# Kernel tuning notes

Hardware: AMD Instinct MI355X
Metric: run time of the kernel (lower is better)

Reference implementation:

```python
import jax, jax.numpy as jnp
import numpy as np

N_HEADS = 16
ROPE_BASE = 10000.0

def apply_rope(x):
    # x: [B, H, S, D] with D even; interleaved-pair RoPE (torchtune style)
    B, H, S, D = x.shape
    half = D // 2
    inv_freq = 1.0 / (ROPE_BASE ** (jnp.arange(0, half, dtype=jnp.float32) / half))
    angles = jnp.arange(S, dtype=jnp.float32)[:, None] * inv_freq[None, :]  # [S, D/2]
    cos = jnp.cos(angles)[None, None]  # [1,1,S,D/2]
    sin = jnp.sin(angles)[None, None]
    x1 = x[..., 0::2]
    x2 = x[..., 1::2]
    r1 = x1 * cos - x2 * sin
    r2 = x1 * sin + x2 * cos
    return jnp.stack([r1, r2], axis=-1).reshape(B, H, S, D)

def setup_inputs() -> dict:
    key = jax.random.key(0)
    ks = jax.random.split(key, 5)
    B, S, E = 2, 2048, 1024
    d_attn = 1024
    scale = 1.0 / np.sqrt(E)
    x = jax.random.normal(ks[0], (B, S, E), dtype=jnp.float32)
    Wq = jax.random.normal(ks[1], (d_attn, E), dtype=jnp.float32) * scale
    Wk = jax.random.normal(ks[2], (d_attn, E), dtype=jnp.float32) * scale
    Wv = jax.random.normal(ks[3], (d_attn, E), dtype=jnp.float32) * scale
    Wo = jax.random.normal(ks[4], (E, d_attn), dtype=jnp.float32) * scale
    return {"x": x, "Wq": Wq, "Wk": Wk, "Wv": Wv, "Wo": Wo}

def reference(x, Wq, Wk, Wv, Wo):
    B, S, E = x.shape
    d_attn = Wq.shape[0]
    hd = d_attn // N_HEADS
    attn_scale = 1.0 / np.sqrt(d_attn)
    # projections (nn.Linear: x @ W.T), split heads -> [B, H, S, hd]
    q = (x @ Wq.T).reshape(B, S, N_HEADS, hd).transpose(0, 2, 1, 3)
    k = (x @ Wk.T).reshape(B, S, N_HEADS, hd).transpose(0, 2, 1, 3)
    v = (x @ Wv.T).reshape(B, S, N_HEADS, hd).transpose(0, 2, 1, 3)
    q = apply_rope(q)
    k = apply_rope(k)
    scores = jnp.einsum('bhqd,bhkd->bhqk', q, k) * attn_scale  # [B,H,S,S]
    causal = jnp.tril(jnp.ones((S, S), dtype=bool))
    scores = jnp.where(causal[None, None], scores, -jnp.inf)
    probs = jax.nn.softmax(scores, axis=-1)  # dropout is identity in eval
    out = jnp.einsum('bhqk,bhkd->bhqd', probs, v)
    out = out.transpose(0, 2, 1, 3).reshape(B, S, d_attn)
    return out @ Wo.T
```

## Files before the change

### kernel.cpp

```cpp
#include <hip/hip_runtime.h>


typedef float  f32x4  __attribute__((ext_vector_type(4)));
typedef short  short8 __attribute__((ext_vector_type(8)));

#define MFMA16(a,b,c) __builtin_amdgcn_mfma_f32_16x16x32_bf16((a),(b),(c),0,0,0)
#define GLD_LDS16(g, l)                                                        \
  __builtin_amdgcn_global_load_lds(                                            \
      (const __attribute__((address_space(1))) unsigned int*)(g),              \
      (__attribute__((address_space(3))) unsigned int*)(l), 16, 0, 0)

__device__ __forceinline__ unsigned short f2bf(float f) {
  unsigned int x = __float_as_uint(f);
  x += 0x7fffu + ((x >> 16) & 1u);
  return (unsigned short)(x >> 16);
}
__device__ __forceinline__ float bf2f(unsigned short u) {
  return __uint_as_float(((unsigned int)u) << 16);
}

__global__ __launch_bounds__(256) void cvt_all(const float* __restrict__ x,
                                               const float* __restrict__ wq,
                                               const float* __restrict__ wk,
                                               const float* __restrict__ wv,
                                               const float* __restrict__ wo,
                                               ushort* __restrict__ dst) {
  const int i = blockIdx.x * 256 + threadIdx.x;
  const float* src;
  int off;
  if (i < 1048576) { src = x; off = i; }
  else {
    const int j = i - 1048576;
    const int wsel = j >> 18;
    off = j & 262143;
    src = (wsel == 0) ? wq : (wsel == 1) ? wk : (wsel == 2) ? wv : wo;
  }
  const float4 v = ((const float4*)src)[off];
  ushort4 o = make_ushort4(f2bf(v.x), f2bf(v.y), f2bf(v.z), f2bf(v.w));
  ((ushort4*)dst)[i] = o;
}

template<int MODE, int BN, int BM>
__global__ __launch_bounds__(256) void gemm_bt(const ushort* __restrict__ A,
                                               const ushort* __restrict__ B,
                                               void* __restrict__ Cv,
                                               int K) {
  constexpr int NI = BN / 32;
  constexpr int MI = BM / 32;
  constexpr int AI = BM / 64;
  constexpr int BI = BN / 64;
  __shared__ __align__(16) short As0[BM * 32];
  __shared__ __align__(16) short As1[BM * 32];
  __shared__ __align__(16) short Bs0[BN * 32];
  __shared__ __align__(16) short Bs1[BN * 32];
  const int tid  = threadIdx.x;
  const int lane = tid & 63, w = tid >> 6;
  const int ln   = lane & 15, quad = lane >> 4;
  const int wm   = w >> 1, wn = w & 1;
  const int m0 = blockIdx.y * BM, n0 = blockIdx.x * BN;

  const int srow = lane >> 2;
  const int schk = (lane & 3) * 8;
  const int arow = w * (16 * AI);
  const int brow = w * (16 * BI);
  const ushort* Ag0 = A + (size_t)(m0 + arow + srow) * K + schk;
  const ushort* Ag1 = A + (size_t)(m0 + arow + 16 + srow) * K + schk;
  const ushort* Bg0 = B + (size_t)(n0 + brow + srow) * K + schk;
  const ushort* Bg1 = B + (size_t)(n0 + brow + 16 + srow) * K + schk;
  const int lA0 = arow * 32, lA1 = (arow + 16) * 32;
  const int lB0 = brow * 32, lB1 = (brow + 16) * 32;

  int aoff[MI], boff[NI];
#pragma unroll
  for (int i = 0; i < MI; i++)
    aoff[i] = (wm * (BM / 2) + i * 16 + ln) * 32 + quad * 8;
#pragma unroll
  for (int i = 0; i < NI; i++)
    boff[i] = (wn * (BN / 2) + i * 16 + ln) * 32 + quad * 8;
  f32x4 acc[MI][NI] = {};

  for (int kt = 0; kt < K; kt += 64) {
    __syncthreads();
    GLD_LDS16(Ag0 + kt, As0 + lA0);
    if (AI == 2) GLD_LDS16(Ag1 + kt, As0 + lA1);
    GLD_LDS16(Ag0 + kt + 32, As1 + lA0);
    if (AI == 2) GLD_LDS16(Ag1 + kt + 32, As1 + lA1);
    GLD_LDS16(Bg0 + kt, Bs0 + lB0);
    if (BI == 2) GLD_LDS16(Bg1 + kt, Bs0 + lB1);
    GLD_LDS16(Bg0 + kt + 32, Bs1 + lB0);
    if (BI == 2) GLD_LDS16(Bg1 + kt + 32, Bs1 + lB1);
    __syncthreads();
#pragma unroll
    for (int h = 0; h < 2; ++h) {
      const short* Ap = h ? As1 : As0;
      const short* Bp = h ? Bs1 : Bs0;
      short8 av[MI], bv[NI];
#pragma unroll
      for (int i = 0; i < MI; i++) av[i] = *(const short8*)&Ap[aoff[i]];
#pragma unroll
      for (int i = 0; i < NI; i++) bv[i] = *(const short8*)&Bp[boff[i]];
#pragma unroll
      for (int mi = 0; mi < MI; mi++)
#pragma unroll
        for (int ni = 0; ni < NI; ni++)
          acc[mi][ni] = MFMA16(av[mi], bv[ni], acc[mi][ni]);
    }
  }

  if (MODE == 0) {
    ushort* Cq = (ushort*)Cv;
    if (n0 < 2048) {
      ushort* dst = Cq + (n0 < 1024 ? 0 : 4194304);
      const int nbase = (n0 < 1024) ? n0 : n0 - 1024;
      const float qsc = (n0 < 1024) ? 0.04508422002778011f : 1.0f;
      const float sgn = (ln & 1) ? 1.0f : -1.0f;
      float invc[NI];
#pragma unroll
      for (int ni = 0; ni < NI; ni++) {
        const int ii = ((wn * (BN / 2) + ni * 16 + ln) & 63) >> 1;
        invc[ni] = __builtin_amdgcn_exp2f(-(float)ii * 0.4152410118579865f) *
                   0.15915494309189535f;
      }
#pragma unroll
      for (int mi = 0; mi < MI; mi++) {
        const int row = m0 + wm * (BM / 2) + mi * 16 + quad * 4;
#pragma unroll
        for (int ni = 0; ni < NI; ni++) {
          const int col = nbase + wn * (BN / 2) + ni * 16 + ln;
#pragma unroll
          for (int r = 0; r < 4; r++) {
            const float mine  = acc[mi][ni][r];
            const float other = __shfl_xor(mine, 1, 64);
            const int   s     = (row + r) & 2047;
            const float rev   = (float)s * invc[ni];
            const float rr    = rev - floorf(rev);
            const float sn = __builtin_amdgcn_sinf(rr);
            const float cs = __builtin_amdgcn_cosf(rr);
            const float rot = (mine * cs + sgn * other * sn) * qsc;
            dst[(size_t)(row + r) * 1024 + col] = f2bf(rot);
          }
        }
      }
    } else {
      ushort* vt = Cq + 8388608;
#pragma unroll
      for (int mi = 0; mi < MI; mi++) {
        const int sm = m0 + wm * (BM / 2) + mi * 16 + quad * 4;
        const int b = sm >> 11, s = sm & 2047;
#pragma unroll
        for (int ni = 0; ni < NI; ni++) {
          const int nv = (n0 - 2048) + wn * (BN / 2) + ni * 16 + ln;
          const int bh = b * 16 + (nv >> 6), d = nv & 63;
          ushort4 u = make_ushort4(f2bf(acc[mi][ni][0]), f2bf(acc[mi][ni][1]),
                                   f2bf(acc[mi][ni][2]), f2bf(acc[mi][ni][3]));
          *(ushort4*)&vt[((size_t)bh * 64 + d) * 2048 + s] = u;
        }
      }
    }
  } else {
    float* C = (float*)Cv;
#pragma unroll
    for (int mi = 0; mi < MI; mi++) {
      const int row = m0 + wm * (BM / 2) + mi * 16 + quad * 4;
#pragma unroll
      for (int ni = 0; ni < NI; ni++) {
        const int col = n0 + wn * (BN / 2) + ni * 16 + ln;
#pragma unroll
        for (int r = 0; r < 4; r++)
          C[(size_t)(row + r) * 1024 + col] = acc[mi][ni][r];
      }
    }
  }
}

__global__ __launch_bounds__(256) void attnk(const ushort* __restrict__ q,
                                             const ushort* __restrict__ k,
                                             const ushort* __restrict__ vt,
                                             ushort* __restrict__ ctx) {
  __shared__ __align__(16) short Ks[64 * 72];
  __shared__ __align__(16) short Vs[64 * 72];
  __shared__ __align__(16) short Ps[4 * 16 * 72];
  const int tid  = threadIdx.x;
  const int lane = tid & 63, w = tid >> 6;
  const int ln   = lane & 15, quad = lane >> 4;
  const int x = blockIdx.x, bh = blockIdx.y;
  const int b = bh >> 4, h = bh & 15;
  const int jA = x, jB = 31 - x;
  short* Pw = Ps + w * 1152;

  const size_t qbA = ((size_t)(b * 2048 + jA * 64 + w * 16 + ln)) * 1024 + h * 64;
  const size_t qbB = ((size_t)(b * 2048 + jB * 64 + w * 16 + ln)) * 1024 + h * 64;
  const short8 aqA0 = *(const short8*)&q[qbA + quad * 8];
  const short8 aqA1 = *(const short8*)&q[qbA + 32 + quad * 8];
  const short8 aqB0 = *(const short8*)&q[qbB + quad * 8];
  const short8 aqB1 = *(const short8*)&q[qbB + 32 + quad * 8];

  f32x4 oA[4] = {}, oB[4] = {};
  float lsA[4] = {0.f, 0.f, 0.f, 0.f}, lsB[4] = {0.f, 0.f, 0.f, 0.f};

  const int s0 = tid, s1 = tid + 256;
  const int r0 = s0 >> 3, c0 = (s0 & 7) * 8;
  const int r1 = s1 >> 3, c1 = (s1 & 7) * 8;
  const ushort* kg0 = k  + ((size_t)(b * 2048 + r0)) * 1024 + h * 64 + c0;
  const ushort* kg1 = k  + ((size_t)(b * 2048 + r1)) * 1024 + h * 64 + c1;
  const ushort* vg0 = vt + ((size_t)(bh * 64 + r0)) * 2048 + c0;
  const ushort* vg1 = vt + ((size_t)(bh * 64 + r1)) * 2048 + c1;
  const int wK0 = r0 * 72 + c0, wK1 = r1 * 72 + c1;

  for (int t = 0; t <= jB; t++) {
    __syncthreads();
    *(short8*)&Ks[wK0] = *(const short8*)(kg0 + (size_t)t * 65536);
    *(short8*)&Ks[wK1] = *(const short8*)(kg1 + (size_t)t * 65536);
    *(short8*)&Vs[wK0] = *(const short8*)(vg0 + t * 64);
    *(short8*)&Vs[wK1] = *(const short8*)(vg1 + t * 64);
    __syncthreads();

    const bool actA = (t <= jA);
    f32x4 scA[4], scB[4];
#pragma unroll
    for (int ct = 0; ct < 4; ct++) {
      const short8 bk0 = *(const short8*)&Ks[(ct * 16 + ln) * 72 + quad * 8];
      const short8 bk1 = *(const short8*)&Ks[(ct * 16 + ln) * 72 + 32 + quad * 8];
      f32x4 z = {0.f, 0.f, 0.f, 0.f};
      z = MFMA16(aqB0, bk0, z);
      z = MFMA16(aqB1, bk1, z);
      scB[ct] = z;
      if (actA) {
        f32x4 y = {0.f, 0.f, 0.f, 0.f};
        y = MFMA16(aqA0, bk0, y);
        y = MFMA16(aqA1, bk1, y);
        scA[ct] = y;
      }
    }
    if (t == jB) {
#pragma unroll
      for (int ct = 0; ct < 4; ct++) {
        const int kv = (t << 6) + ct * 16 + ln;
#pragma unroll
        for (int r = 0; r < 4; r++)
          if (kv > jB * 64 + w * 16 + quad * 4 + r) scB[ct][r] = -100000.0f;
      }
    }
    if (actA && t == jA) {
#pragma unroll
      for (int ct = 0; ct < 4; ct++) {
        const int kv = (t << 6) + ct * 16 + ln;
#pragma unroll
        for (int r = 0; r < 4; r++)
          if (kv > jA * 64 + w * 16 + quad * 4 + r) scA[ct][r] = -100000.0f;
      }
    }

    short8 bv0[4], bv1[4];
#pragma unroll
    for (int dt = 0; dt < 4; dt++) {
      bv0[dt] = *(const short8*)&Vs[(dt * 16 + ln) * 72 + quad * 8];
      bv1[dt] = *(const short8*)&Vs[(dt * 16 + ln) * 72 + 32 + quad * 8];
    }

#pragma unroll
    for (int ct = 0; ct < 4; ct++)
#pragma unroll
      for (int r = 0; r < 4; r++) {
        const float p = __builtin_amdgcn_exp2f(scB[ct][r]);
        lsB[r] += p;
        Pw[(quad * 4 + r) * 72 + ct * 16 + ln] = (short)f2bf(p);
      }
    {
      const short8 ap0 = *(const short8*)&Pw[ln * 72 + quad * 8];
      const short8 ap1 = *(const short8*)&Pw[ln * 72 + 32 + quad * 8];
#pragma unroll
      for (int dt = 0; dt < 4; dt++) {
        oB[dt] = MFMA16(ap0, bv0[dt], oB[dt]);
        oB[dt] = MFMA16(ap1, bv1[dt], oB[dt]);
      }
    }
    if (actA) {
#pragma unroll
      for (int ct = 0; ct < 4; ct++)
#pragma unroll
        for (int r = 0; r < 4; r++) {
          const float p = __builtin_amdgcn_exp2f(scA[ct][r]);
          lsA[r] += p;
          Pw[(quad * 4 + r) * 72 + ct * 16 + ln] = (short)f2bf(p);
        }
      const short8 ap0 = *(const short8*)&Pw[ln * 72 + quad * 8];
      const short8 ap1 = *(const short8*)&Pw[ln * 72 + 32 + quad * 8];
#pragma unroll
      for (int dt = 0; dt < 4; dt++) {
        oA[dt] = MFMA16(ap0, bv0[dt], oA[dt]);
        oA[dt] = MFMA16(ap1, bv1[dt], oA[dt]);
      }
    }
  }

#pragma unroll
  for (int off = 1; off < 16; off <<= 1)
#pragma unroll
    for (int r = 0; r < 4; r++) {
      lsA[r] += __shfl_xor(lsA[r], off, 64);
      lsB[r] += __shfl_xor(lsB[r], off, 64);
    }

#pragma unroll
  for (int r = 0; r < 4; r++) {
    const float invA = 1.0f / lsA[r];
    const float invB = 1.0f / lsB[r];
    const int rowA = jA * 64 + w * 16 + quad * 4 + r;
    const int rowB = jB * 64 + w * 16 + quad * 4 + r;
#pragma unroll
    for (int dt = 0; dt < 4; dt++) {
      ctx[((size_t)(b * 2048 + rowA)) * 1024 + h * 64 + dt * 16 + ln] =
          f2bf(oA[dt][r] * invA);
      ctx[((size_t)(b * 2048 + rowB)) * 1024 + h * 64 + dt * 16 + ln] =
          f2bf(oB[dt][r] * invB);
    }
  }
}

extern "C" void kernel_launch(void* const* d_in, const int* in_sizes, int n_in,
                              void* d_out, int out_size, void* d_ws, size_t ws_size,
                              hipStream_t stream) {
  const float* x  = (const float*)d_in[0];
  const float* Wq = (const float*)d_in[1];
  const float* Wk = (const float*)d_in[2];
  const float* Wv = (const float*)d_in[3];
  const float* Wo = (const float*)d_in[4];
  float* out = (float*)d_out;
  char* ws = (char*)d_ws;

  ushort* xb  = (ushort*)(ws);
  ushort* wqb = (ushort*)(ws + (size_t)(8  << 20));
  ushort* qb  = (ushort*)(ws + (size_t)(16 << 20));
  ushort* kb  = (ushort*)(ws + (size_t)(24 << 20));
  ushort* vtb = (ushort*)(ws + (size_t)(32 << 20));
  ushort* ctx = (ushort*)(ws + (size_t)(40 << 20));

  cvt_all<<<8192, 256, 0, stream>>>(x, Wq, Wk, Wv, Wo, xb);
  gemm_bt<0, 64, 128><<<dim3(48, 32), 256, 0, stream>>>(xb, wqb, (void*)qb, 1024);
  attnk<<<dim3(16, 32), 256, 0, stream>>>(qb, kb, vtb, ctx);
  gemm_bt<2, 64, 64><<<dim3(16, 64), 256, 0, stream>>>(ctx, wqb + 3145728 , (void*)out, 1024);
}
```

Baseline: 190.8 us.

## Split attention query tiles across 8 waves with double-buffered K/V staging

The attention kernel now launches 512 threads per block, and each group of 4 waves owns one of the two paired query tiles, where before every wave processed both tiles in turn. K/V tiles are double-buffered in LDS and prefetched two steps ahead through registers, which removes one barrier per iteration. QK^T is computed transposed so probabilities pack into bf16 pairs with v_cvt_pk_bf16 and vector LDS stores, and the row-sum reduction needs fewer shuffles. The cost is more LDS per block and idle waves in the short tile during later iterations.

```diff
diff --git a/kernel.cpp b/kernel.cpp
--- a/kernel.cpp
+++ b/kernel.cpp
@@ -17,6 +17,11 @@
 }
 __device__ __forceinline__ float bf2f(unsigned short u) {
   return __uint_as_float(((unsigned int)u) << 16);
+}
+__device__ __forceinline__ unsigned int cvtpk_bf16(float lo, float hi) {
+  unsigned int r;
+  asm("v_cvt_pk_bf16_f32 %0, %1, %2" : "=v"(r) : "v"(lo), "v"(hi));
+  return r;
 }
 
 __global__ __launch_bounds__(256) void cvt_all(const float* __restrict__ x,
@@ -173,147 +178,120 @@
   }
 }
 
-__global__ __launch_bounds__(256) void attnk(const ushort* __restrict__ q,
+__global__ __launch_bounds__(512) void attnk(const ushort* __restrict__ q,
                                              const ushort* __restrict__ k,
                                              const ushort* __restrict__ vt,
                                              ushort* __restrict__ ctx) {
-  __shared__ __align__(16) short Ks[64 * 72];
-  __shared__ __align__(16) short Vs[64 * 72];
-  __shared__ __align__(16) short Ps[4 * 16 * 72];
+  __shared__ __align__(16) short Ks[2][64 * 72];
+  __shared__ __align__(16) short Vs[2][64 * 72];
+  __shared__ __align__(16) short Ps[8 * 16 * 72];
   const int tid  = threadIdx.x;
   const int lane = tid & 63, w = tid >> 6;
   const int ln   = lane & 15, quad = lane >> 4;
   const int x = blockIdx.x, bh = blockIdx.y;
   const int b = bh >> 4, h = bh & 15;
   const int jA = x, jB = 31 - x;
+  const int tile = w >> 2;
+  const int wq   = w & 3;
+  const int j    = tile ? jA : jB;
   short* Pw = Ps + w * 1152;
 
-  const size_t qbA = ((size_t)(b * 2048 + jA * 64 + w * 16 + ln)) * 1024 + h * 64;
-  const size_t qbB = ((size_t)(b * 2048 + jB * 64 + w * 16 + ln)) * 1024 + h * 64;
-  const short8 aqA0 = *(const short8*)&q[qbA + quad * 8];
-  const short8 aqA1 = *(const short8*)&q[qbA + 32 + quad * 8];
-  const short8 aqB0 = *(const short8*)&q[qbB + quad * 8];
-  const short8 aqB1 = *(const short8*)&q[qbB + 32 + quad * 8];
-
-  f32x4 oA[4] = {}, oB[4] = {};
-  float lsA[4] = {0.f, 0.f, 0.f, 0.f}, lsB[4] = {0.f, 0.f, 0.f, 0.f};
-
-  const int s0 = tid, s1 = tid + 256;
-  const int r0 = s0 >> 3, c0 = (s0 & 7) * 8;
-  const int r1 = s1 >> 3, c1 = (s1 & 7) * 8;
-  const ushort* kg0 = k  + ((size_t)(b * 2048 + r0)) * 1024 + h * 64 + c0;
-  const ushort* kg1 = k  + ((size_t)(b * 2048 + r1)) * 1024 + h * 64 + c1;
-  const ushort* vg0 = vt + ((size_t)(bh * 64 + r0)) * 2048 + c0;
-  const ushort* vg1 = vt + ((size_t)(bh * 64 + r1)) * 2048 + c1;
-  const int wK0 = r0 * 72 + c0, wK1 = r1 * 72 + c1;
+  const size_t qb = ((size_t)(b * 2048 + j * 64 + wq * 16 + ln)) * 1024 + h * 64;
+  const short8 aq0 = *(const short8*)&q[qb + quad * 8];
+  const short8 aq1 = *(const short8*)&q[qb + 32 + quad * 8];
+
+  f32x4 o[4] = {};
+  float ls0 = 0.f, ls1 = 0.f;
+
+  const int r0 = tid >> 3, c0 = (tid & 7) * 8;
+  const ushort* kg = k  + ((size_t)(b * 2048 + r0)) * 1024 + h * 64 + c0;
+  const ushort* vg = vt + ((size_t)(bh * 64 + r0)) * 2048 + c0;
+  const int wK = r0 * 72 + c0;
+
+  short8 kr = *(const short8*)(kg);
+  short8 vr = *(const short8*)(vg);
+  *(short8*)&Ks[0][wK] = kr;
+  *(short8*)&Vs[0][wK] = vr;
+  kr = *(const short8*)(kg + 65536);
+  vr = *(const short8*)(vg + 64);
+
+  const int qloc = j * 64 + wq * 16 + ln;
 
   for (int t = 0; t <= jB; t++) {
     __syncthreads();
-    *(short8*)&Ks[wK0] = *(const short8*)(kg0 + (size_t)t * 65536);
-    *(short8*)&Ks[wK1] = *(const short8*)(kg1 + (size_t)t * 65536);
-    *(short8*)&Vs[wK0] = *(const short8*)(vg0 + t * 64);
-    *(short8*)&Vs[wK1] = *(const short8*)(vg1 + t * 64);
-    __syncthreads();
-
-    const bool actA = (t <= jA);
-    f32x4 scA[4], scB[4];
-#pragma unroll
-    for (int ct = 0; ct < 4; ct++) {
-      const short8 bk0 = *(const short8*)&Ks[(ct * 16 + ln) * 72 + quad * 8];
-      const short8 bk1 = *(const short8*)&Ks[(ct * 16 + ln) * 72 + 32 + quad * 8];
-      f32x4 z = {0.f, 0.f, 0.f, 0.f};
-      z = MFMA16(aqB0, bk0, z);
-      z = MFMA16(aqB1, bk1, z);
-      scB[ct] = z;
-      if (actA) {
-        f32x4 y = {0.f, 0.f, 0.f, 0.f};
-        y = MFMA16(aqA0, bk0, y);
-        y = MFMA16(aqA1, bk1, y);
-        scA[ct] = y;
-      }
-    }
-    if (t == jB) {
+    const short* Kc = Ks[t & 1];
+    const short* Vc = Vs[t & 1];
+    if (t < jB) {
+      *(short8*)&Ks[(t & 1) ^ 1][wK] = kr;
+      *(short8*)&Vs[(t & 1) ^ 1][wK] = vr;
+    }
+    if (t + 2 <= jB) {
+      kr = *(const short8*)(kg + (size_t)(t + 2) * 65536);
+      vr = *(const short8*)(vg + (t + 2) * 64);
+    }
+
+    const bool act = (tile == 0) || (t <= jA);
+    if (act) {
+      f32x4 sc[4];
 #pragma unroll
       for (int ct = 0; ct < 4; ct++) {
-        const int kv = (t << 6) + ct * 16 + ln;
-#pragma unroll
-        for (int r = 0; r < 4; r++)
-          if (kv > jB * 64 + w * 16 + quad * 4 + r) scB[ct][r] = -100000.0f;
-      }
-    }
-    if (actA && t == jA) {
+        const short8 bk0 = *(const short8*)&Kc[(ct * 16 + ln) * 72 + quad * 8];
+        const short8 bk1 = *(const short8*)&Kc[(ct * 16 + ln) * 72 + 32 + quad * 8];
+        f32x4 z = {0.f, 0.f, 0.f, 0.f};
+        z = MFMA16(bk0, aq0, z);
+        z = MFMA16(bk1, aq1, z);
+        sc[ct] = z;
+      }
+      if (t == j) {
+#pragma unroll
+        for (int ct = 0; ct < 4; ct++) {
+          const int kvb = (t << 6) + ct * 16 + quad * 4;
+#pragma unroll
+          for (int r = 0; r < 4; r++)
+            if (kvb + r > qloc) sc[ct][r] = -100000.0f;
+        }
+      }
+
+      short8 bv0[4], bv1[4];
+#pragma unroll
+      for (int dt = 0; dt < 4; dt++) {
+        bv0[dt] = *(const short8*)&Vc[(dt * 16 + ln) * 72 + quad * 8];
+        bv1[dt] = *(const short8*)&Vc[(dt * 16 + ln) * 72 + 32 + quad * 8];
+      }
+
 #pragma unroll
       for (int ct = 0; ct < 4; ct++) {
-        const int kv = (t << 6) + ct * 16 + ln;
-#pragma unroll
-        for (int r = 0; r < 4; r++)
-          if (kv > jA * 64 + w * 16 + quad * 4 + r) scA[ct][r] = -100000.0f;
-      }
-    }
-
-    short8 bv0[4], bv1[4];
-#pragma unroll
-    for (int dt = 0; dt < 4; dt++) {
-      bv0[dt] = *(const short8*)&Vs[(dt * 16 + ln) * 72 + quad * 8];
-      bv1[dt] = *(const short8*)&Vs[(dt * 16 + ln) * 72 + 32 + quad * 8];
-    }
-
-#pragma unroll
-    for (int ct = 0; ct < 4; ct++)
-#pragma unroll
-      for (int r = 0; r < 4; r++) {
-        const float p = __builtin_amdgcn_exp2f(scB[ct][r]);
-        lsB[r] += p;
-        Pw[(quad * 4 + r) * 72 + ct * 16 + ln] = (short)f2bf(p);
-      }
-    {
+        const float p0 = __builtin_amdgcn_exp2f(sc[ct][0]);
+        const float p1 = __builtin_amdgcn_exp2f(sc[ct][1]);
+        const float p2 = __builtin_amdgcn_exp2f(sc[ct][2]);
+        const float p3 = __builtin_amdgcn_exp2f(sc[ct][3]);
+        ls0 += p0 + p1;
+        ls1 += p2 + p3;
+        const uint2 u = make_uint2(cvtpk_bf16(p0, p1), cvtpk_bf16(p2, p3));
+        *(uint2*)&Pw[ln * 72 + ct * 16 + quad * 4] = u;
+      }
       const short8 ap0 = *(const short8*)&Pw[ln * 72 + quad * 8];
       const short8 ap1 = *(const short8*)&Pw[ln * 72 + 32 + quad * 8];
 #pragma unroll
       for (int dt = 0; dt < 4; dt++) {
-        oB[dt] = MFMA16(ap0, bv0[dt], oB[dt]);
-        oB[dt] = MFMA16(ap1, bv1[dt], oB[dt]);
-      }
-    }
-    if (actA) {
-#pragma unroll
-      for (int ct = 0; ct < 4; ct++)
-#pragma unroll
-        for (int r = 0; r < 4; r++) {
-          const float p = __builtin_amdgcn_exp2f(scA[ct][r]);
-          lsA[r] += p;
-          Pw[(quad * 4 + r) * 72 + ct * 16 + ln] = (short)f2bf(p);
-        }
-      const short8 ap0 = *(const short8*)&Pw[ln * 72 + quad * 8];
-      const short8 ap1 = *(const short8*)&Pw[ln * 72 + 32 + quad * 8];
-#pragma unroll
-      for (int dt = 0; dt < 4; dt++) {
-        oA[dt] = MFMA16(ap0, bv0[dt], oA[dt]);
-        oA[dt] = MFMA16(ap1, bv1[dt], oA[dt]);
-      }
-    }
-  }
-
-#pragma unroll
-  for (int off = 1; off < 16; off <<= 1)
-#pragma unroll
-    for (int r = 0; r < 4; r++) {
-      lsA[r] += __shfl_xor(lsA[r], off, 64);
-      lsB[r] += __shfl_xor(lsB[r], off, 64);
-    }
+        o[dt] = MFMA16(ap0, bv0[dt], o[dt]);
+        o[dt] = MFMA16(ap1, bv1[dt], o[dt]);
+      }
+    }
+  }
+
+  float l = ls0 + ls1;
+  l += __shfl_xor(l, 16, 64);
+  l += __shfl_xor(l, 32, 64);
 
 #pragma unroll
   for (int r = 0; r < 4; r++) {
-    const float invA = 1.0f / lsA[r];
-    const float invB = 1.0f / lsB[r];
-    const int rowA = jA * 64 + w * 16 + quad * 4 + r;
-    const int rowB = jB * 64 + w * 16 + quad * 4 + r;
+    const float inv = 1.0f / __shfl(l, quad * 4 + r, 64);
+    const int row = j * 64 + wq * 16 + quad * 4 + r;
 #pragma unroll
     for (int dt = 0; dt < 4; dt++) {
-      ctx[((size_t)(b * 2048 + rowA)) * 1024 + h * 64 + dt * 16 + ln] =
-          f2bf(oA[dt][r] * invA);
-      ctx[((size_t)(b * 2048 + rowB)) * 1024 + h * 64 + dt * 16 + ln] =
-          f2bf(oB[dt][r] * invB);
+      ctx[((size_t)(b * 2048 + row)) * 1024 + h * 64 + dt * 16 + ln] =
+          f2bf(o[dt][r] * inv);
     }
   }
 }
@@ -338,6 +316,6 @@
 
   cvt_all<<<8192, 256, 0, stream>>>(x, Wq, Wk, Wv, Wo, xb);
   gemm_bt<0, 64, 128><<<dim3(48, 32), 256, 0, stream>>>(xb, wqb, (void*)qb, 1024);
-  attnk<<<dim3(16, 32), 256, 0, stream>>>(qb, kb, vtb, ctx);
+  attnk<<<dim3(16, 32), 512, 0, stream>>>(qb, kb, vtb, ctx);
   gemm_bt<2, 64, 64><<<dim3(16, 64), 256, 0, stream>>>(ctx, wqb + 3145728 , (void*)out, 1024);
 }
```

New measurement: 175.1 us. 8.2% less time.
